# Kernel optimization log

Hardware: AMD Instinct MI355X
Metric: run time of the kernel (lower is better)

The kernel has to match this reference:

```python
import jax, jax.numpy as jnp
from jax import lax
import numpy as np
import math

B, N, M, SIG, HID, NFEAT, OUT, H = 256, 512, 16, 256, 256, 3, 10, 256
ALPHA, BETA = 1.0, 0.5


def setup_inputs() -> dict:
    key = jax.random.key(0)
    ks = jax.random.split(key, 12)
    s_g = 1.0 / math.sqrt(HID)
    s_f = 1.0 / math.sqrt(SIG)
    return {
        "x": jax.random.normal(ks[0], (B, 1, H, H), jnp.float32),
        "unif": jax.random.uniform(ks[1], (B, N), jnp.float32),
        "z": jax.random.normal(ks[2], (B, N, 2), jnp.float32),
        "m_g_params": jax.random.normal(ks[3], (1, 6 * M), jnp.float32),
        "gc1_w": jax.random.uniform(ks[4], (NFEAT, HID), jnp.float32, -s_g, s_g),
        "gc1_b": jax.random.uniform(ks[5], (HID,), jnp.float32, -s_g, s_g),
        "gc2_w": jax.random.uniform(ks[6], (HID, HID), jnp.float32, -s_g, s_g),
        "gc2_b": jax.random.uniform(ks[7], (HID,), jnp.float32, -s_g, s_g),
        "collapser1": 0.1 * jax.random.normal(ks[8], (SIG, N), jnp.float32),
        "collapser2": 0.1 * jax.random.normal(ks[9], (SIG, N), jnp.float32),
        "fcf_w": jax.random.uniform(ks[10], (OUT, SIG), jnp.float32, -s_f, s_f),
        "fcf_b": jax.random.uniform(ks[11], (OUT,), jnp.float32, -s_f, s_f),
    }


def _mixture_fields(m_g_params):
    # torch: split [num_sample, 6M] into M chunks of 6, stack -> [M, N, 6],
    # split along last dim, then .view(N, M) in C-order on the [M, N] field.
    raw = m_g_params.reshape(M, 6)  # [M, 6]
    return [jnp.broadcast_to(raw[:, j][:, None], (M, N)).reshape(N, M) for j in range(6)]


def reference(x, unif, z, m_g_params, gc1_w, gc1_b, gc2_w, gc2_b,
              collapser1, collapser2, fcf_w, fcf_b):
    pi_f, mux_f, muy_f, sx_f, sy_f, rho_f = _mixture_fields(m_g_params)
    pi = jax.nn.softmax(pi_f, axis=-1)            # [N, M]
    # categorical sampling via CDF inversion, vectorized over batch
    cdf = jnp.cumsum(pi, axis=-1)                 # [N, M]
    idx = jnp.argmax(unif[:, :, None] < cdf[None], axis=-1)  # [B, N]
    row = jnp.arange(N)[None, :]
    gat = lambda f: f[row, idx]                   # [B, N]
    mux, muy = gat(mux_f), gat(muy_f)
    sx, sy = jnp.exp(gat(sx_f)), jnp.exp(gat(sy_f))
    rho = jnp.tanh(gat(rho_f))
    # reparameterized bivariate-normal sample via Cholesky (lower)
    z1, z2 = z[..., 0], z[..., 1]
    xs = mux + sx * z1
    ys = muy + sy * (rho * z1 + jnp.sqrt(1.0 - rho * rho) * z2)
    # torch MVN.sample() is no_grad -> detach samples
    xs_c, ys_c = lax.stop_gradient(xs), lax.stop_gradient(ys)
    dx, dy = xs_c - mux, ys_c - muy
    omr2 = 1.0 - rho * rho
    quad = (dx * dx / (sx * sx) - 2.0 * rho * dx * dy / (sx * sy) + dy * dy / (sy * sy)) / omr2
    logprob = (-jnp.log(2.0 * jnp.pi) - jnp.log(sx * sy)
               - 0.5 * jnp.log(omr2) - 0.5 * quad)  # [B, N]
    full_log_prob = logprob.sum(axis=-1)           # [B]
    loc = jnp.tanh(jnp.stack([xs_c, ys_c], axis=-1))  # [B, N, 2]
    # adjacency: inverse shifted pairwise squared distance
    diff = loc[:, :, None, :] - loc[:, None, :, :]  # [B, N, N, 2]
    adj = 1.0 / (ALPHA + BETA * jnp.sum(diff * diff, axis=-1))  # [B, N, N]
    # pixel gather: denormalize (trunc toward zero, like torch .long())
    pix = jnp.trunc(0.5 * (loc + 1.0) * H - 0.1).astype(jnp.int32)
    pix = jnp.clip(pix, 0, H - 1)
    bidx = jnp.arange(B)[:, None]
    pv = x[bidx, :, pix[..., 0], pix[..., 1]]      # [B, N, 1]
    feat = jnp.concatenate([pv, loc], axis=-1)     # [B, N, 3]
    # GCN (eval mode: no dropout)
    s1 = jax.nn.relu(jnp.einsum('bnm,bmh->bnh', adj, feat @ gc1_w) + gc1_b)
    s2 = jax.nn.relu(jnp.einsum('bnm,bmh->bnh', adj, s1 @ gc2_w) + gc2_b)
    # nn.Softmax() (no dim) on 3D input resolves to dim=0 in torch
    g1 = jax.nn.softmax(jnp.einsum('sn,bnh->bsh', collapser1, s1), axis=0)
    g2 = jax.nn.softmax(jnp.einsum('sn,bnh->bsh', collapser2, s2), axis=0)
    sig = (g1 + g2).sum(axis=2)                    # [B, SIG]
    out = jax.nn.softmax(sig @ fcf_w.T + fcf_b, axis=-1)  # [B, OUT]
    return out, full_log_prob
```

## Files before the change

### kernel.cpp

```cpp
#include <hip/hip_runtime.h>
#include <hip/hip_bf16.h>
#include <math.h>

#define Bx   256
#define Nx   512
#define SIGx 256
#define HIDx 256
#define OUTx 10
#define Hx   256

typedef __attribute__((ext_vector_type(4))) float f32x4;
typedef long fp8x8;
typedef unsigned char uchar;

__device__ inline uchar f2fp8(float v) {
    int r = __builtin_amdgcn_cvt_pk_fp8_f32(v, 0.0f, 0, false);
    return (uchar)(r & 0xff);
}
__device__ inline uint pk4fp8(float a0, float a1, float a2, float a3) {
    int r = __builtin_amdgcn_cvt_pk_fp8_f32(a0, a1, 0, false);
    r = __builtin_amdgcn_cvt_pk_fp8_f32(a2, a3, r, true);
    return (uint)r;
}

__device__ inline void gload_lds16(const uchar* g, uchar* l) {
    __builtin_amdgcn_global_load_lds(
        (const __attribute__((address_space(1))) uint*)g,
        (__attribute__((address_space(3))) uint*)l, 16, 0, 0);
}
__device__ inline const uchar* laddr(const uchar* base, int row, int kb) {
    int ps = (kb >> 4) ^ ((row >> 1) & 3) ^ ((row >> 4) & 3);
    return base + row*64 + ps*16 + (kb & 15);
}

__global__ __launch_bounds__(512) void kA_sample(
    const float* __restrict__ x, const float* __restrict__ z,
    const float* __restrict__ mg, float* __restrict__ feat,
    float* __restrict__ flp)
{
    int b = blockIdx.x;
    int n = threadIdx.x;
    int g = n >> 5;
    float mux = mg[g*6+1];
    float muy = mg[g*6+2];
    float sxv = expf(mg[g*6+3]);
    float syv = expf(mg[g*6+4]);
    float rho = tanhf(mg[g*6+5]);
    float z1 = z[((size_t)b*Nx + n)*2 + 0];
    float z2 = z[((size_t)b*Nx + n)*2 + 1];
    float omr2 = 1.0f - rho*rho;
    float xs = mux + sxv*z1;
    float ys = muy + syv*(rho*z1 + sqrtf(omr2)*z2);
    float dx = xs - mux, dy = ys - muy;
    float quad = (dx*dx/(sxv*sxv) - 2.0f*rho*dx*dy/(sxv*syv) + dy*dy/(syv*syv)) / omr2;
    float logprob = -1.8378770664093453f - logf(sxv*syv) - 0.5f*logf(omr2) - 0.5f*quad;
    float lx = tanhf(xs), ly = tanhf(ys);
    int px = (int)truncf(0.5f*(lx+1.0f)*(float)Hx - 0.1f);
    int py = (int)truncf(0.5f*(ly+1.0f)*(float)Hx - 0.1f);
    px = px < 0 ? 0 : (px > Hx-1 ? Hx-1 : px);
    py = py < 0 ? 0 : (py > Hx-1 ? Hx-1 : py);
    float pv = x[(size_t)b*Hx*Hx + (size_t)px*Hx + py];
    size_t fo = ((size_t)b*Nx + n)*3;
    feat[fo+0] = pv; feat[fo+1] = lx; feat[fo+2] = ly;

    __shared__ float red[512];
    red[n] = logprob;
    __syncthreads();
    for (int st = 256; st > 0; st >>= 1) {
        if (n < st) red[n] += red[n+st];
        __syncthreads();
    }
    if (n == 0) flp[b] = red[0];
}

__global__ __launch_bounds__(256) void kPrep(
    const float* __restrict__ c1, const float* __restrict__ c2,
    const float* __restrict__ w2,
    uchar* __restrict__ c1q, uchar* __restrict__ c2q, uchar* __restrict__ w2tq)
{
    int idx = blockIdx.x*256 + threadIdx.x;
    if (idx < SIGx*Nx) {
        c1q[idx] = f2fp8(16.0f * c1[idx]);
        c2q[idx] = f2fp8(16.0f * c2[idx]);
    }
    if (idx < HIDx*HIDx) {
        int i = idx >> 8, j = idx & 255;
        w2tq[idx] = f2fp8(16.0f * w2[j*HIDx + i]);
    }
}

__global__ __launch_bounds__(512) void kFuse1(
    const float* __restrict__ featL, const float* __restrict__ w1,
    const float* __restrict__ b1,
    f32x4* __restrict__ locpL, uchar* __restrict__ s1tAll)
{
    int b = blockIdx.x;
    const float* fb = featL + (size_t)b*Nx*3;
    f32x4* locb = locpL + (size_t)b*Nx;
    uchar* s1t = s1tAll + (size_t)b*HIDx*Nx;

    __shared__ float fpv[Nx], flx[Nx], fly[Nx], fH[Nx];
    __shared__ float w1s[3*HIDx], b1s[HIDx];
    __shared__ float Gp[4][3][Nx];

    int t = threadIdx.x;
    {
        float pv = fb[t*3+0], lx = fb[t*3+1], ly = fb[t*3+2];
        fpv[t] = pv; flx[t] = lx; fly[t] = ly;
        float hx = fmaf(0.5f*lx, lx, fmaf(0.5f*ly, ly, 1.0f));
        fH[t] = hx;
        locb[t] = (f32x4){lx, ly, hx, fmaf(0.5f*lx, lx, 0.5f*ly*ly)};
    }
    for (int i = t; i < 3*HIDx; i += 512) w1s[i] = w1[i];
    if (t < HIDx) b1s[t] = b1[t];
    __syncthreads();

    int tq = t & 127;
    int mc = t >> 7;
    int n4 = tq*4;

    float xn[4], yn[4], cn[4];
    #pragma unroll
    for (int e = 0; e < 4; ++e) {
        xn[e] = flx[n4+e]; yn[e] = fly[n4+e];
        cn[e] = fmaf(0.5f*xn[e], xn[e], 0.5f*yn[e]*yn[e]);
    }
    float G0[4] = {}, G1[4] = {}, G2[4] = {};

    int m0 = mc*128;
    #pragma unroll 4
    for (int mm = 0; mm < 128; ++mm) {
        int m = m0 + mm;
        float hx = fH[m], fx = flx[m], fy = fly[m];
        float a[4];
        #pragma unroll
        for (int e = 0; e < 4; ++e) {
            float s = fmaf(-yn[e], fy, fmaf(-xn[e], fx, hx + cn[e]));
            a[e] = __builtin_amdgcn_rcpf(s);
            G0[e] = fmaf(a[e], fpv[m], G0[e]);
            G1[e] = fmaf(a[e], fx, G1[e]);
            G2[e] = fmaf(a[e], fy, G2[e]);
        }
    }

    *(f32x4*)&Gp[mc][0][n4] = (f32x4){G0[0],G0[1],G0[2],G0[3]};
    *(f32x4*)&Gp[mc][1][n4] = (f32x4){G1[0],G1[1],G1[2],G1[3]};
    *(f32x4*)&Gp[mc][2][n4] = (f32x4){G2[0],G2[1],G2[2],G2[3]};
    __syncthreads();

    f32x4 T0 = {}, T1 = {}, T2 = {};
    #pragma unroll
    for (int j = 0; j < 4; ++j) {
        T0 += *(const f32x4*)&Gp[j][0][n4];
        T1 += *(const f32x4*)&Gp[j][1][n4];
        T2 += *(const f32x4*)&Gp[j][2][n4];
    }

    int hc = mc;
    #pragma unroll 4
    for (int hh = 0; hh < 64; ++hh) {
        int h = hc*64 + hh;
        float w0 = w1s[h], wA = w1s[HIDx+h], wB = w1s[2*HIDx+h], bb = b1s[h];
        float v0 = fminf(fmaxf(fmaf(T0.x,w0, fmaf(T1.x,wA, fmaf(T2.x,wB, bb))), 0.0f), 448.0f);
        float v1 = fminf(fmaxf(fmaf(T0.y,w0, fmaf(T1.y,wA, fmaf(T2.y,wB, bb))), 0.0f), 448.0f);
        float v2 = fminf(fmaxf(fmaf(T0.z,w0, fmaf(T1.z,wA, fmaf(T2.z,wB, bb))), 0.0f), 448.0f);
        float v3 = fminf(fmaxf(fmaf(T0.w,w0, fmaf(T1.w,wA, fmaf(T2.w,wB, bb))), 0.0f), 448.0f);
        *(uint*)(s1t + (size_t)h*Nx + n4) = pk4fp8(v0, v1, v2, v3);
    }
}

__global__ __launch_bounds__(256) void kGemmAdjR(
    const uchar* __restrict__ Aall, const f32x4* __restrict__ locp,
    const float* __restrict__ bias, uchar* __restrict__ outAll)
{
    int b    = blockIdx.x;
    int tile = blockIdx.y;
    int rt = tile >> 2;
    int ct = tile & 3;
    const uchar* A = Aall + (size_t)b*HIDx*Nx;
    const f32x4* locB = locp + (size_t)b*Nx;
    uchar* outp = outAll + (size_t)b*HIDx*Nx;

    __shared__ __align__(16) uchar Als[128*64];
    __shared__ __align__(16) uchar Bls[128*72];
    int t = threadIdx.x;
    int lane = t & 63, wave = t >> 6;
    int wr = wave >> 1, wc = wave & 1;
    int q = lane >> 4, c16 = lane & 15;
    int r0 = rt*128, n0 = ct*128;
    int lrow = lane >> 2;
    int pu   = lane & 3;

    int row = t & 127;
    int kb0 = __builtin_amdgcn_readfirstlane((t >> 7) * 32);
    f32x4 nd = locB[n0 + row];
    float xn = nd.x, yn = nd.y, cnv = nd.w;
    uchar* brow = Bls + row*72;

    f32x4 acc[4][4] = {};

    for (int kk = 0; kk < Nx; kk += 64) {
        #pragma unroll
        for (int r = 0; r < 2; ++r) {
            int chunk = wave*2 + r;
            int srow = chunk*16 + lrow;
            int sl = pu ^ ((srow>>1)&3) ^ ((srow>>4)&3);
            gload_lds16(A + (size_t)(r0+srow)*Nx + kk + sl*16, Als + chunk*1024);
        }
        const f32x4* mp = locB + kk + kb0;
        #pragma unroll
        for (int i = 0; i < 8; ++i) {
            f32x4 m0 = mp[i*4+0], m1 = mp[i*4+1], m2 = mp[i*4+2], m3 = mp[i*4+3];
            float s0 = fmaf(-yn, m0.y, fmaf(-xn, m0.x, m0.z + cnv));
            float s1 = fmaf(-yn, m1.y, fmaf(-xn, m1.x, m1.z + cnv));
            float s2 = fmaf(-yn, m2.y, fmaf(-xn, m2.x, m2.z + cnv));
            float s3 = fmaf(-yn, m3.y, fmaf(-xn, m3.x, m3.z + cnv));
            *(uint*)(brow + kb0 + i*4) = pk4fp8(
                __builtin_amdgcn_rcpf(s0), __builtin_amdgcn_rcpf(s1),
                __builtin_amdgcn_rcpf(s2), __builtin_amdgcn_rcpf(s3));
        }
        __syncthreads();
        #pragma unroll
        for (int ks = 0; ks < 64; ks += 32) {
            fp8x8 af[4], bfr[4];
            #pragma unroll
            for (int i = 0; i < 4; ++i)
                af[i] = *(const fp8x8*)laddr(Als, wr*64 + i*16 + c16, ks + q*8);
            #pragma unroll
            for (int j = 0; j < 4; ++j)
                bfr[j] = *(const fp8x8*)(Bls + (size_t)(wc*64 + j*16 + c16)*72 + ks + q*8);
            #pragma unroll
            for (int i = 0; i < 4; ++i)
                #pragma unroll
                for (int j = 0; j < 4; ++j)
                    acc[i][j] = __builtin_amdgcn_mfma_f32_16x16x32_fp8_fp8(af[i], bfr[j], acc[i][j], 0, 0, 0);
        }
        __syncthreads();
    }
    #pragma unroll
    for (int i = 0; i < 4; ++i) {
        int rowb = r0 + wr*64 + i*16 + q*4;
        #pragma unroll
        for (int j = 0; j < 4; ++j) {
            int col = n0 + wc*64 + j*16 + c16;
            #pragma unroll
            for (int r = 0; r < 4; ++r) {
                float v = fmaxf(acc[i][j][r] + bias[rowb + r], 0.0f) * 0.25f;
                outp[(size_t)(rowb + r)*Nx + col] = f2fp8(fminf(v, 448.0f));
            }
        }
    }
}

template<int K, int NC, bool TRB>
__global__ __launch_bounds__(256) void kGstdQ(
    const uchar* __restrict__ Ash, const uchar* __restrict__ Ball,
    uchar* __restrict__ outAll, float oscale)
{
    constexpr int CT = NC / 128;
    int b    = blockIdx.x;
    int tile = blockIdx.y;
    int rt = tile / CT;
    int ct = tile % CT;
    const uchar* B = Ball + (size_t)b*HIDx*Nx;
    uchar* outp = outAll + (size_t)b*HIDx*NC;

    __shared__ __align__(16) uchar Als[128*64];
    __shared__ __align__(16) uchar Bls[128*64];
    int t = threadIdx.x;
    int lane = t & 63, wave = t >> 6;
    int wr = wave >> 1, wc = wave & 1;
    int q = lane >> 4, c16 = lane & 15;
    int r0 = rt*128, n0 = ct*128;
    int lrow = lane >> 2;
    int pu   = lane & 3;
    f32x4 acc[4][4] = {};

    for (int kk = 0; kk < K; kk += 64) {
        #pragma unroll
        for (int r = 0; r < 2; ++r) {
            int chunk = wave*2 + r;
            int row = chunk*16 + lrow;
            int sl = pu ^ ((row>>1)&3) ^ ((row>>4)&3);
            gload_lds16(Ash + (size_t)(r0+row)*K + kk + sl*16, Als + chunk*1024);
            if (!TRB)
                gload_lds16(B + (size_t)(n0+row)*K + kk + sl*16, Bls + chunk*1024);
        }
        if (TRB) {
            int pi  = t & 31;
            int nc8 = t >> 5;
            int hk = kk + 2*pi;
            const uchar* g0 = B + (size_t)hk*NC + n0 + nc8*16;
            const uchar* g1 = g0 + NC;
            float4 v0 = *(const float4*)g0;
            float4 v1 = *(const float4*)g1;
            const uchar* pa = (const uchar*)&v0;
            const uchar* qa = (const uchar*)&v1;
            int kb = 2*pi;
            int s  = kb >> 4;
            #pragma unroll
            for (int e = 0; e < 16; ++e) {
                int row = nc8*16 + e;
                int ps = s ^ ((row>>1)&3) ^ ((row>>4)&3);
                *(ushort*)(Bls + row*64 + ps*16 + (kb & 15)) =
                    (ushort)pa[e] | ((ushort)qa[e] << 8);
            }
        }
        __syncthreads();
        #pragma unroll
        for (int ks = 0; ks < 64; ks += 32) {
            fp8x8 af[4], bfr[4];
            #pragma unroll
            for (int i = 0; i < 4; ++i)
                af[i] = *(const fp8x8*)laddr(Als, wr*64 + i*16 + c16, ks + q*8);
            #pragma unroll
            for (int j = 0; j < 4; ++j)
                bfr[j] = *(const fp8x8*)laddr(Bls, wc*64 + j*16 + c16, ks + q*8);
            #pragma unroll
            for (int i = 0; i < 4; ++i)
                #pragma unroll
                for (int j = 0; j < 4; ++j)
                    acc[i][j] = __builtin_amdgcn_mfma_f32_16x16x32_fp8_fp8(af[i], bfr[j], acc[i][j], 0, 0, 0);
        }
        __syncthreads();
    }
    #pragma unroll
    for (int i = 0; i < 4; ++i) {
        int rowb = r0 + wr*64 + i*16 + q*4;
        #pragma unroll
        for (int j = 0; j < 4; ++j) {
            int col = n0 + wc*64 + j*16 + c16;
            #pragma unroll
            for (int r = 0; r < 4; ++r) {
                float v = acc[i][j][r] * oscale;
                v = fminf(fmaxf(v, -448.0f), 448.0f);
                outp[(size_t)(rowb + r)*NC + col] = f2fp8(v);
            }
        }
    }
}

__global__ __launch_bounds__(512) void kF1q(
    const uchar* __restrict__ t1, const uchar* __restrict__ t2,
    float* __restrict__ m1, float* __restrict__ rd1,
    float* __restrict__ m2, float* __restrict__ rd2)
{
    int s = blockIdx.x;
    int t = threadIdx.x;
    int hq = t & 63;
    int bq = t >> 6;
    const size_t str = (size_t)SIGx*HIDx;
    size_t base = (size_t)(bq*32)*str + (size_t)s*HIDx + hq*4;

    float mv1[4], dv1[4], mv2[4], dv2[4];
    #pragma unroll
    for (int e = 0; e < 4; ++e) { mv1[e]=-3.0e38f; dv1[e]=0.0f; mv2[e]=-3.0e38f; dv2[e]=0.0f; }

    for (int i = 0; i < 32; ++i) {
        uint u1 = *(const uint*)(t1 + base + (size_t)i*str);
        uint u2 = *(const uint*)(t2 + base + (size_t)i*str);
        float v1[4], v2[4];
        v1[0] = __builtin_amdgcn_cvt_f32_fp8(u1, 0);
        v1[1] = __builtin_amdgcn_cvt_f32_fp8(u1, 1);
        v1[2] = __builtin_amdgcn_cvt_f32_fp8(u1, 2);
        v1[3] = __builtin_amdgcn_cvt_f32_fp8(u1, 3);
        v2[0] = __builtin_amdgcn_cvt_f32_fp8(u2, 0);
        v2[1] = __builtin_amdgcn_cvt_f32_fp8(u2, 1);
        v2[2] = __builtin_amdgcn_cvt_f32_fp8(u2, 2);
        v2[3] = __builtin_amdgcn_cvt_f32_fp8(u2, 3);
        #pragma unroll
        for (int e = 0; e < 4; ++e) {
            float mn;
            mn = fmaxf(mv1[e], v1[e]);
            dv1[e] = dv1[e]*__expf(mv1[e]-mn) + __expf(v1[e]-mn); mv1[e] = mn;
            mn = fmaxf(mv2[e], v2[e]);
            dv2[e] = dv2[e]*__expf(mv2[e]-mn) + __expf(v2[e]-mn); mv2[e] = mn;
        }
    }

    __shared__ float pm1[8][256], pd1[8][256], pm2[8][256], pd2[8][256];
    #pragma unroll
    for (int e = 0; e < 4; ++e) {
        pm1[bq][hq*4+e] = mv1[e]; pd1[bq][hq*4+e] = dv1[e];
        pm2[bq][hq*4+e] = mv2[e]; pd2[bq][hq*4+e] = dv2[e];
    }
    __syncthreads();

    if (t < 256) {
        int h = t;
        float m = -3.0e38f, d = 0.0f;
        #pragma unroll
        for (int j = 0; j < 8; ++j) {
            float mm = pm1[j][h], dd = pd1[j][h];
            float mn = fmaxf(m, mm);
            d = d*__expf(m-mn) + dd*__expf(mm-mn);
            m = mn;
        }
        size_t o = (size_t)s*HIDx + h;
        m1[o] = m; rd1[o] = 1.0f/d;
    } else {
        int h = t - 256;
        float m = -3.0e38f, d = 0.0f;
        #pragma unroll
        for (int j = 0; j < 8; ++j) {
            float mm = pm2[j][h], dd = pd2[j][h];
            float mn = fmaxf(m, mm);
            d = d*__expf(m-mn) + dd*__expf(mm-mn);
            m = mn;
        }
        size_t o = (size_t)s*HIDx + h;
        m2[o] = m; rd2[o] = 1.0f/d;
    }
}

__global__ __launch_bounds__(256) void kF2q(
    const uchar* __restrict__ t1, const uchar* __restrict__ t2,
    const float* __restrict__ m1, const float* __restrict__ rd1,
    const float* __restrict__ m2, const float* __restrict__ rd2,
    float* __restrict__ sig)
{
    int b = blockIdx.y;
    int sq = threadIdx.x >> 6;
    int s = blockIdx.x*4 + sq;
    int hq = threadIdx.x & 63;
    size_t sh = (size_t)s*HIDx + hq*4;
    size_t tb = ((size_t)b*SIGx + s)*HIDx + hq*4;
    uint u1 = *(const uint*)(t1 + tb);
    uint u2 = *(const uint*)(t2 + tb);
    f32x4 a1 = *(const f32x4*)&m1[sh];
    f32x4 r1 = *(const f32x4*)&rd1[sh];
    f32x4 a2 = *(const f32x4*)&m2[sh];
    f32x4 r2 = *(const f32x4*)&rd2[sh];
    float v = 0.0f;
    v += __expf(__builtin_amdgcn_cvt_f32_fp8(u1,0) - a1.x) * r1.x;
    v += __expf(__builtin_amdgcn_cvt_f32_fp8(u1,1) - a1.y) * r1.y;
    v += __expf(__builtin_amdgcn_cvt_f32_fp8(u1,2) - a1.z) * r1.z;
    v += __expf(__builtin_amdgcn_cvt_f32_fp8(u1,3) - a1.w) * r1.w;
    v += __expf(__builtin_amdgcn_cvt_f32_fp8(u2,0) - a2.x) * r2.x;
    v += __expf(__builtin_amdgcn_cvt_f32_fp8(u2,1) - a2.y) * r2.y;
    v += __expf(__builtin_amdgcn_cvt_f32_fp8(u2,2) - a2.z) * r2.z;
    v += __expf(__builtin_amdgcn_cvt_f32_fp8(u2,3) - a2.w) * r2.w;

    __shared__ float red[256];
    red[threadIdx.x] = v;
    __syncthreads();
    for (int st = 32; st > 0; st >>= 1) {
        if (hq < st) red[threadIdx.x] += red[threadIdx.x + st];
        __syncthreads();
    }
    if (hq == 0) sig[(size_t)b*SIGx + s] = red[sq*64];
}

__global__ __launch_bounds__(256) void kG_out(
    const float* __restrict__ sig, const float* __restrict__ fw,
    const float* __restrict__ fb, float* __restrict__ out)
{
    int b = blockIdx.x;
    int tid = threadIdx.x;
    __shared__ float red[256];
    __shared__ float logits[OUTx];
    float sv = sig[(size_t)b*SIGx + tid];
    for (int o = 0; o < OUTx; ++o) {
        red[tid] = sv * fw[o*SIGx + tid];
        __syncthreads();
        for (int st = 128; st > 0; st >>= 1) {
            if (tid < st) red[tid] += red[tid+st];
            __syncthreads();
        }
        if (tid == 0) logits[o] = red[0] + fb[o];
        __syncthreads();
    }
    if (tid == 0) {
        float mx = logits[0];
        for (int o = 1; o < OUTx; ++o) mx = fmaxf(mx, logits[o]);
        float dd = 0.0f; float e[OUTx];
        for (int o = 0; o < OUTx; ++o) { e[o] = expf(logits[o]-mx); dd += e[o]; }
        float inv = 1.0f/dd;
        for (int o = 0; o < OUTx; ++o) out[(size_t)b*OUTx + o] = e[o]*inv;
    }
}

static inline size_t alignup(size_t b) { return (b + 255) & ~(size_t)255; }

extern "C" void kernel_launch(void* const* d_in, const int* in_sizes, int n_in,
                              void* d_out, int out_size, void* d_ws, size_t ws_size,
                              hipStream_t stream)
{
    const float* x   = (const float*)d_in[0];
    const float* z   = (const float*)d_in[2];
    const float* mg  = (const float*)d_in[3];
    const float* w1  = (const float*)d_in[4];
    const float* b1  = (const float*)d_in[5];
    const float* w2  = (const float*)d_in[6];
    const float* b2  = (const float*)d_in[7];
    const float* c1  = (const float*)d_in[8];
    const float* c2  = (const float*)d_in[9];
    const float* fw  = (const float*)d_in[10];
    const float* fbv = (const float*)d_in[11];
    float* out = (float*)d_out;
    float* flp = out + (size_t)Bx*OUTx;
    (void)in_sizes; (void)n_in; (void)out_size;

    char* ws = (char*)d_ws;
    size_t off = 0;
    auto alloc = [&](size_t bytes) -> char* {
        char* p = ws + off; off += alignup(bytes); return p;
    };
    float*  feat = (float*)alloc((size_t)Bx*Nx*3*4);
    f32x4*  locp = (f32x4*)alloc((size_t)Bx*Nx*16);
    uchar*  c1q  = (uchar*)alloc((size_t)SIGx*Nx);
    uchar*  c2q  = (uchar*)alloc((size_t)SIGx*Nx);
    uchar*  w2tq = (uchar*)alloc((size_t)HIDx*HIDx);
    uchar*  t1   = (uchar*)alloc((size_t)Bx*SIGx*HIDx);
    uchar*  t2   = (uchar*)alloc((size_t)Bx*SIGx*HIDx);
    float*  m1   = (float*)alloc((size_t)SIGx*HIDx*4);
    float*  d1   = (float*)alloc((size_t)SIGx*HIDx*4);
    float*  m2   = (float*)alloc((size_t)SIGx*HIDx*4);
    float*  d2   = (float*)alloc((size_t)SIGx*HIDx*4);
    float*  sig  = (float*)alloc((size_t)Bx*SIGx*4);
    size_t fixed = off;

    int BC = 1;
    for (int c = Bx; c >= 1; c >>= 1) {
        size_t need = fixed + 2*alignup((size_t)c*HIDx*Nx);
        if (need <= ws_size) { BC = c; break; }
    }
    uchar* P1   = (uchar*)alloc((size_t)BC*HIDx*Nx);
    uchar* P2   = (uchar*)alloc((size_t)BC*HIDx*Nx);

    hipLaunchKernelGGL(kA_sample, dim3(Bx), dim3(Nx), 0, stream, x, z, mg, feat, flp);
    hipLaunchKernelGGL(kPrep, dim3(512), dim3(256), 0, stream, c1, c2, w2, c1q, c2q, w2tq);

    const int nch = Bx / BC;
    for (int c = 0; c < nch; ++c) {
        int b0 = c * BC;
        const float* featL = feat + (size_t)b0*Nx*3;
        f32x4* locpL = locp + (size_t)b0*Nx;
        uchar* t1L = t1 + (size_t)b0*SIGx*HIDx;
        uchar* t2L = t2 + (size_t)b0*SIGx*HIDx;
        hipLaunchKernelGGL(kFuse1, dim3(BC), dim3(512), 0, stream,
                           featL, w1, b1, locpL, P2);
        hipLaunchKernelGGL((kGstdQ<512,256,false>), dim3(BC, 4), dim3(256), 0, stream,
                           c1q, P2, t1L, 0.0625f);
        hipLaunchKernelGGL((kGstdQ<256,512,true>), dim3(BC, 8), dim3(256), 0, stream,
                           w2tq, P2, P1, 0.0625f);
        hipLaunchKernelGGL(kGemmAdjR, dim3(BC, 8), dim3(256), 0, stream,
                           P1, locpL, b2, P2);
        hipLaunchKernelGGL((kGstdQ<512,256,false>), dim3(BC, 4), dim3(256), 0, stream,
                           c2q, P2, t2L, 0.25f);
    }

    hipLaunchKernelGGL(kF1q, dim3(SIGx), dim3(512), 0, stream,
                       t1, t2, m1, d1, m2, d2);
    hipLaunchKernelGGL(kF2q, dim3(SIGx/4, Bx), dim3(256), 0, stream,
                       t1, t2, m1, d1, m2, d2, sig);
    hipLaunchKernelGGL(kG_out, dim3(Bx), dim3(256), 0, stream, sig, fw, fbv, out);
}
```

Measured before the change: 302.9 us.

## Cover all 256 rows per block and double-buffer adjacency GEMM stages

The adjacency GEMM kernel now computes all 256 output rows per block (two 128-row subtiles), so the recomputed fp8 adjacency tile is built once per column tile instead of twice. It also double-buffers the A and B shared-memory tiles and interleaves the next stage's global loads and adjacency recomputation with the current MFMAs, leaving one barrier per k-step. In exchange the grid halves to 4 column tiles per batch, and accumulator registers and LDS use double, which may cut occupancy.

```diff
diff --git a/kernel.cpp b/kernel.cpp
--- a/kernel.cpp
+++ b/kernel.cpp
@@ -169,25 +169,23 @@
     }
 }
 
-__global__ __launch_bounds__(256) void kGemmAdjR(
+__global__ __launch_bounds__(256) void kGemmAdjM(
     const uchar* __restrict__ Aall, const f32x4* __restrict__ locp,
     const float* __restrict__ bias, uchar* __restrict__ outAll)
 {
-    int b    = blockIdx.x;
-    int tile = blockIdx.y;
-    int rt = tile >> 2;
-    int ct = tile & 3;
+    int b  = blockIdx.x;
+    int ct = blockIdx.y;
     const uchar* A = Aall + (size_t)b*HIDx*Nx;
     const f32x4* locB = locp + (size_t)b*Nx;
     uchar* outp = outAll + (size_t)b*HIDx*Nx;
 
-    __shared__ __align__(16) uchar Als[128*64];
-    __shared__ __align__(16) uchar Bls[128*72];
+    __shared__ __align__(16) uchar Als[2][256*64];
+    __shared__ __align__(16) uchar Bls[2][128*72];
     int t = threadIdx.x;
     int lane = t & 63, wave = t >> 6;
     int wr = wave >> 1, wc = wave & 1;
     int q = lane >> 4, c16 = lane & 15;
-    int r0 = rt*128, n0 = ct*128;
+    int n0 = ct*128;
     int lrow = lane >> 2;
     int pu   = lane & 3;
 
@@ -195,19 +193,21 @@
     int kb0 = __builtin_amdgcn_readfirstlane((t >> 7) * 32);
     f32x4 nd = locB[n0 + row];
     float xn = nd.x, yn = nd.y, cnv = nd.w;
-    uchar* brow = Bls + row*72;
-
-    f32x4 acc[4][4] = {};
-
-    for (int kk = 0; kk < Nx; kk += 64) {
-        #pragma unroll
-        for (int r = 0; r < 2; ++r) {
-            int chunk = wave*2 + r;
+
+    f32x4 acc[2][4][4] = {};
+
+    auto stageA = [&](int buf, int kkv) {
+        #pragma unroll
+        for (int r = 0; r < 4; ++r) {
+            int chunk = wave*4 + r;
             int srow = chunk*16 + lrow;
             int sl = pu ^ ((srow>>1)&3) ^ ((srow>>4)&3);
-            gload_lds16(A + (size_t)(r0+srow)*Nx + kk + sl*16, Als + chunk*1024);
-        }
-        const f32x4* mp = locB + kk + kb0;
+            gload_lds16(A + (size_t)srow*Nx + kkv + sl*16, Als[buf] + chunk*1024);
+        }
+    };
+    auto recompB = [&](int buf, int kkv) {
+        const f32x4* mp = locB + kkv + kb0;
+        uchar* brow = Bls[buf] + row*72;
         #pragma unroll
         for (int i = 0; i < 8; ++i) {
             f32x4 m0 = mp[i*4+0], m1 = mp[i*4+1], m2 = mp[i*4+2], m3 = mp[i*4+3];
@@ -219,37 +219,60 @@
                 __builtin_amdgcn_rcpf(s0), __builtin_amdgcn_rcpf(s1),
                 __builtin_amdgcn_rcpf(s2), __builtin_amdgcn_rcpf(s3));
         }
-        __syncthreads();
-        #pragma unroll
-        for (int ks = 0; ks < 64; ks += 32) {
-            fp8x8 af[4], bfr[4];
+    };
+    auto mfmaHalf = [&](int buf, int ks) {
+        const uchar* Ac = Als[buf];
+        const uchar* Bc = Bls[buf];
+        fp8x8 bfr[4];
+        #pragma unroll
+        for (int j = 0; j < 4; ++j)
+            bfr[j] = *(const fp8x8*)(Bc + (size_t)(wc*64 + j*16 + c16)*72 + ks + q*8);
+        #pragma unroll
+        for (int rt = 0; rt < 2; ++rt) {
+            fp8x8 af[4];
             #pragma unroll
             for (int i = 0; i < 4; ++i)
-                af[i] = *(const fp8x8*)laddr(Als, wr*64 + i*16 + c16, ks + q*8);
-            #pragma unroll
-            for (int j = 0; j < 4; ++j)
-                bfr[j] = *(const fp8x8*)(Bls + (size_t)(wc*64 + j*16 + c16)*72 + ks + q*8);
+                af[i] = *(const fp8x8*)laddr(Ac, rt*128 + wr*64 + i*16 + c16, ks + q*8);
             #pragma unroll
             for (int i = 0; i < 4; ++i)
                 #pragma unroll
                 for (int j = 0; j < 4; ++j)
-                    acc[i][j] = __builtin_amdgcn_mfma_f32_16x16x32_fp8_fp8(af[i], bfr[j], acc[i][j], 0, 0, 0);
-        }
-        __syncthreads();
-    }
+                    acc[rt][i][j] = __builtin_amdgcn_mfma_f32_16x16x32_fp8_fp8(
+                        af[i], bfr[j], acc[rt][i][j], 0, 0, 0);
+        }
+    };
+
+    stageA(0, 0);
+    recompB(0, 0);
+    __syncthreads();
+
+    int cur = 0;
+    for (int kk = 0; kk < Nx; kk += 64) {
+        int nxt = cur ^ 1;
+        bool more = (kk + 64) < Nx;
+        if (more) stageA(nxt, kk + 64);
+        mfmaHalf(cur, 0);
+        if (more) recompB(nxt, kk + 64);
+        mfmaHalf(cur, 32);
+        __syncthreads();
+        cur = nxt;
+    }
+
     #pragma unroll
-    for (int i = 0; i < 4; ++i) {
-        int rowb = r0 + wr*64 + i*16 + q*4;
-        #pragma unroll
-        for (int j = 0; j < 4; ++j) {
-            int col = n0 + wc*64 + j*16 + c16;
-            #pragma unroll
-            for (int r = 0; r < 4; ++r) {
-                float v = fmaxf(acc[i][j][r] + bias[rowb + r], 0.0f) * 0.25f;
-                outp[(size_t)(rowb + r)*Nx + col] = f2fp8(fminf(v, 448.0f));
+    for (int rt = 0; rt < 2; ++rt)
+        #pragma unroll
+        for (int i = 0; i < 4; ++i) {
+            int rowb = rt*128 + wr*64 + i*16 + q*4;
+            #pragma unroll
+            for (int j = 0; j < 4; ++j) {
+                int col = n0 + wc*64 + j*16 + c16;
+                #pragma unroll
+                for (int r = 0; r < 4; ++r) {
+                    float v = fmaxf(acc[rt][i][j][r] + bias[rowb + r], 0.0f) * 0.25f;
+                    outp[(size_t)(rowb + r)*Nx + col] = f2fp8(fminf(v, 448.0f));
+                }
             }
         }
-    }
 }
 
 template<int K, int NC, bool TRB>
@@ -544,7 +567,7 @@
                            c1q, P2, t1L, 0.0625f);
         hipLaunchKernelGGL((kGstdQ<256,512,true>), dim3(BC, 8), dim3(256), 0, stream,
                            w2tq, P2, P1, 0.0625f);
-        hipLaunchKernelGGL(kGemmAdjR, dim3(BC, 8), dim3(256), 0, stream,
+        hipLaunchKernelGGL(kGemmAdjM, dim3(BC, 4), dim3(256), 0, stream,
                            P1, locpL, b2, P2);
         hipLaunchKernelGGL((kGstdQ<512,256,false>), dim3(BC, 4), dim3(256), 0, stream,
                            c2q, P2, t2L, 0.25f);
```

Result: slower. 354.3 us (+17.0%).
